# Kernel optimization log

Hardware: AMD Instinct MI355X
Metric: run time of the kernel (lower is better)

Reference implementation:

```python
import jax, jax.numpy as jnp
import numpy as np
from collections import defaultdict

H = 24; W = 24          # patch grid
B0 = 64                 # original batch (len(batch_id))
B = 128                 # total batch incl. augmented copies
C_IN = 256; HID = 128; HEADS_S = 2; OUT = 256; K = 9; NCLS = 8


def _build_space_edges():
    # knn_graph on the normalized meshgrid coords; identical for every image -> offset copies.
    P = H * W
    coords = np.stack(np.meshgrid(np.arange(H), np.arange(W), indexing='ij'), -1).reshape(-1, 2).astype(np.float32)
    cn = coords / coords.max()
    d = ((cn[:, None, :] - cn[None, :, :]) ** 2).sum(-1)
    np.fill_diagonal(d, np.inf)              # loop=False
    nbr = np.argsort(d, axis=1)[:, :K]       # [P, K] neighbor (source) ids
    off = (np.arange(B0) * P)[:, None, None]
    src = (nbr[None] + off).reshape(-1)
    dst = (np.broadcast_to(np.arange(P)[:, None], (P, K))[None] + off).reshape(-1)
    return np.stack([src, dst]).astype(np.int64)


def _build_view_edges(bid_all):
    groups = defaultdict(list)
    for i, c in enumerate(bid_all.tolist()):
        groups[c].append(i)
    ei = []
    for c, mem in groups.items():
        for a in range(len(mem)):
            for b in range(a + 1, len(mem)):
                i, j = mem[a], mem[b]
                if i >= B0 and j >= B0:
                    continue               # skip augmented-augmented pairs
                ei.append((i, j)); ei.append((j, i))
    return np.array(ei, dtype=np.int64).T


def setup_inputs() -> dict:
    key = jax.random.key(0)
    ks = jax.random.split(key, 8)
    bid = np.repeat(np.arange(NCLS), B0 // NCLS).astype(np.int64)
    bid_all = np.concatenate([bid, bid])
    s = 0.05
    return {
        'x': jax.random.normal(ks[0], (B, C_IN, H, W), jnp.float32),
        'batch_id_all': jnp.asarray(bid_all),
        'batch_id': jnp.asarray(bid),
        'edge_index_space': jnp.asarray(_build_space_edges()),
        'edge_index_view': jnp.asarray(_build_view_edges(bid_all)),
        'W_space': jax.random.normal(ks[1], (C_IN, HEADS_S * HID), jnp.float32) * s,
        'att_src_space': jax.random.normal(ks[2], (HEADS_S, HID), jnp.float32) * s,
        'att_dst_space': jax.random.normal(ks[3], (HEADS_S, HID), jnp.float32) * s,
        'bias_space': jnp.zeros((HEADS_S * HID,), jnp.float32),
        'W_view': jax.random.normal(ks[4], (HEADS_S * HID, OUT), jnp.float32) * s,
        'att_src_view': jax.random.normal(ks[5], (1, OUT), jnp.float32) * s,
        'att_dst_view': jax.random.normal(ks[6], (1, OUT), jnp.float32) * s,
        'bias_view': jnp.zeros((OUT,), jnp.float32),
    }


def _gat(xn, edges, Wm, a_src, a_dst, bias, heads, outc):
    # PyG GATConv: linear -> per-edge leaky_relu attn -> segment softmax over dst -> scatter-add
    N = xn.shape[0]
    loops = jnp.arange(N, dtype=edges.dtype)              # add_self_loops=True
    src = jnp.concatenate([edges[0], loops])
    dst = jnp.concatenate([edges[1], loops])
    h = (xn @ Wm).reshape(N, heads, outc)                 # [N, H, C]
    a_s = jnp.sum(h * a_src[None], -1)                    # [N, H]
    a_d = jnp.sum(h * a_dst[None], -1)
    e = jax.nn.leaky_relu(a_s[src] + a_d[dst], 0.2)       # [E, H]
    m = jax.ops.segment_max(e, dst, num_segments=N)
    ee = jnp.exp(e - m[dst])
    ssum = jax.ops.segment_sum(ee, dst, num_segments=N)
    alpha = ee / (ssum[dst] + 1e-16)
    out = jax.ops.segment_sum(h[src] * alpha[..., None], dst, num_segments=N)
    return out.reshape(N, heads * outc) + bias            # concat=True


def reference(x, batch_id_all, batch_id, edge_index_space, edge_index_view,
              W_space, att_src_space, att_dst_space, bias_space,
              W_view, att_src_view, att_dst_view, bias_view):
    P = H * W
    node = x[:B0].transpose(0, 2, 3, 1).reshape(-1, C_IN)                # [B0*P, C_in]
    x_space = _gat(node, edge_index_space, W_space, att_src_space,
                   att_dst_space, bias_space, HEADS_S, HID)              # [B0*P, 256]
    emb = x_space.reshape(B0, P, -1).mean(axis=1)                        # per-image mean pool
    emb_all = emb[jnp.arange(B) % B0]                                    # augmented i -> i % B0
    feat = _gat(emb_all, edge_index_view, W_view, att_src_view,
                att_dst_view, bias_view, 1, OUT)                         # [B, 256]
    C = feat.shape[1]
    x_view = 0.5 * x_space.reshape(B0, P, C) + 0.5 * feat[:B0][:, None, :]
    # torch does .reshape(-1, C).view(B, C, H, W): a raw row-major reinterpret
    return x_view.reshape(B0, C, H, W)
```

## Files before the change

### kernel.cpp

```cpp
#include <hip/hip_runtime.h>

#define PGRID 576
#define NB0   64
#define CIN   256
#define KNN   9
#define NNODE (NB0 * PGRID)

typedef __attribute__((ext_vector_type(8))) short short8;
typedef __attribute__((ext_vector_type(4))) float f32x4;

__device__ __forceinline__ float bf2f(unsigned short u) {
    union { unsigned int i; float f; } v; v.i = ((unsigned int)u) << 16; return v.f;
}
__device__ __forceinline__ unsigned short f2b(float f) {
    unsigned int u = __float_as_uint(f);
    return (unsigned short)((u + 0x7FFFu + ((u >> 16) & 1u)) >> 16);
}

__global__ __launch_bounds__(256) void prep_w(const float* __restrict__ W,
                                              unsigned short* __restrict__ Wt) {
    __shared__ float tile[64][65];
    const int c0 = blockIdx.x * 64, j0 = blockIdx.y * 64;
    const int t = threadIdx.x, lo = t % 64, hi = t / 64;
#pragma unroll
    for (int r = 0; r < 16; ++r)
        tile[r * 4 + hi][lo] = W[(size_t)(c0 + r * 4 + hi) * 256 + j0 + lo];
    __syncthreads();
#pragma unroll
    for (int r = 0; r < 16; ++r)
        Wt[(size_t)(j0 + r * 4 + hi) * 256 + c0 + lo] = f2b(tile[lo][r * 4 + hi]);
}

__global__ __launch_bounds__(256) void gemm_fused(
    const float* __restrict__ x, const unsigned short* __restrict__ Wt,
    const float* __restrict__ att_src, const float* __restrict__ att_dst,
    unsigned short* __restrict__ h, float* __restrict__ as_, float* __restrict__ ad_) {
    const int bx = blockIdx.x;
    const int t  = threadIdx.x;
    const int b  = bx / 9;
    const int p0 = (bx % 9) * 64;
    const int n0 = bx * 64;
    const int l = t & 63, w = t >> 6;
    const int l4 = l >> 4, l15 = l & 15;
    const float* xb = x + (size_t)b * (CIN * PGRID);
    const int prow = p0 + w * 16 + l15;

    float a0[64];
#pragma unroll
    for (int cq = 0; cq < 8; ++cq)
#pragma unroll
        for (int jj = 0; jj < 8; ++jj) {
            int c = cq * 32 + l4 * 8 + jj;
            a0[cq * 8 + jj] = xb[(size_t)c * PGRID + prow];
        }
    short8 apk[8];
#pragma unroll
    for (int cq = 0; cq < 8; ++cq) {
        short8 v;
#pragma unroll
        for (int jj = 0; jj < 8; ++jj) v[jj] = (short)f2b(a0[cq * 8 + jj]);
        apk[cq] = v;
    }

    f32x4 acc[16] = {};
    const unsigned short* wbase = Wt + (size_t)l15 * 256 + l4 * 8;
#pragma unroll
    for (int q = 0; q < 8; ++q) {
#pragma unroll
        for (int f = 0; f < 16; ++f) {
            short8 wf = *(const short8*)(wbase + (size_t)f * 4096 + q * 32);
            acc[f] = __builtin_amdgcn_mfma_f32_16x16x32_bf16(wf, apk[q], acc[f], 0, 0, 0);
        }
    }

    unsigned short* hrow = h + (size_t)(n0 + w * 16 + l15) * 256 + l4 * 4;
#pragma unroll
    for (int f = 0; f < 16; ++f) {
        uint2 pk;
        pk.x = (unsigned int)f2b(acc[f][0]) | ((unsigned int)f2b(acc[f][1]) << 16);
        pk.y = (unsigned int)f2b(acc[f][2]) | ((unsigned int)f2b(acc[f][3]) << 16);
        *(uint2*)(hrow + f * 16) = pk;
    }

    float s0 = 0.f, s1 = 0.f, d0 = 0.f, d1 = 0.f;
#pragma unroll
    for (int f = 0; f < 16; ++f) {
        float4 av = *(const float4*)(att_src + f * 16 + l4 * 4);
        float4 dv = *(const float4*)(att_dst + f * 16 + l4 * 4);
        float ss = acc[f][0] * av.x + acc[f][1] * av.y + acc[f][2] * av.z + acc[f][3] * av.w;
        float dd = acc[f][0] * dv.x + acc[f][1] * dv.y + acc[f][2] * dv.z + acc[f][3] * dv.w;
        if (f < 8) { s0 += ss; d0 += dd; } else { s1 += ss; d1 += dd; }
    }
    s0 += __shfl_xor(s0, 16); s0 += __shfl_xor(s0, 32);
    s1 += __shfl_xor(s1, 16); s1 += __shfl_xor(s1, 32);
    d0 += __shfl_xor(d0, 16); d0 += __shfl_xor(d0, 32);
    d1 += __shfl_xor(d1, 16); d1 += __shfl_xor(d1, 32);
    if (l < 16) {
        int n = n0 + w * 16 + l;
        float2 sv; sv.x = s0; sv.y = s1;
        float2 dv2; dv2.x = d0; dv2.y = d1;
        *(float2*)(as_ + 2 * n) = sv;
        *(float2*)(ad_ + 2 * n) = dv2;
    }
}

__global__ __launch_bounds__(256) void space_gather(
    const unsigned short* __restrict__ h, const float* __restrict__ as_,
    const float* __restrict__ ad_, const int* __restrict__ esrc,
    const float* __restrict__ bias, unsigned short* __restrict__ xsb) {
    const int t = threadIdx.x;
    const int g = t >> 6, l = t & 63;
    const int n = blockIdx.x * 4 + g;
    int srcs[10];
#pragma unroll
    for (int k = 0; k < 9; ++k) srcs[k] = esrc[n * 9 + k];
    srcs[9] = n;
    const int head = l >> 5;
    const float adv = ad_[n * 2 + head];
    float e[10];
    float m = -1e30f;
#pragma unroll
    for (int k = 0; k < 10; ++k) {
        float ev = as_[srcs[k] * 2 + head] + adv;
        ev = ev >= 0.f ? ev : 0.2f * ev;
        e[k] = ev; m = fmaxf(m, ev);
    }
    float ssum = 0.f;
#pragma unroll
    for (int k = 0; k < 10; ++k) { e[k] = __expf(e[k] - m); ssum += e[k]; }
    const float inv = 1.f / (ssum + 1e-16f);
    const int j4 = l * 4;
    float o0 = 0.f, o1 = 0.f, o2 = 0.f, o3 = 0.f;
#pragma unroll
    for (int k = 0; k < 10; ++k) {
        uint2 v = *(const uint2*)(h + (size_t)srcs[k] * 256 + j4);
        o0 += e[k] * bf2f((unsigned short)(v.x & 0xffff));
        o1 += e[k] * bf2f((unsigned short)(v.x >> 16));
        o2 += e[k] * bf2f((unsigned short)(v.y & 0xffff));
        o3 += e[k] * bf2f((unsigned short)(v.y >> 16));
    }
    float4 bi = *(const float4*)(bias + j4);
    o0 = o0 * inv + bi.x; o1 = o1 * inv + bi.y;
    o2 = o2 * inv + bi.z; o3 = o3 * inv + bi.w;
    uint2 pk;
    pk.x = (unsigned int)f2b(o0) | ((unsigned int)f2b(o1) << 16);
    pk.y = (unsigned int)f2b(o2) | ((unsigned int)f2b(o3) << 16);
    *(uint2*)(xsb + (size_t)n * 256 + j4) = pk;
}

__global__ __launch_bounds__(256) void pool_partial(const unsigned short* __restrict__ xsb,
                                                    float* __restrict__ embp) {
    __shared__ float red[4][256];
    const int b = blockIdx.x, seg = blockIdx.y;
    const int t = threadIdx.x;
    const int l = t & 63, sub = t >> 6;
    const int j4 = l * 4;
    const unsigned short* base = xsb + ((size_t)b * PGRID + seg * 64 + sub * 16) * 256 + j4;
    float s0 = 0.f, s1 = 0.f, s2 = 0.f, s3 = 0.f;
#pragma unroll
    for (int p = 0; p < 16; ++p) {
        uint2 v = *(const uint2*)(base + (size_t)p * 256);
        s0 += bf2f((unsigned short)(v.x & 0xffff));
        s1 += bf2f((unsigned short)(v.x >> 16));
        s2 += bf2f((unsigned short)(v.y & 0xffff));
        s3 += bf2f((unsigned short)(v.y >> 16));
    }
    float4 sv; sv.x = s0; sv.y = s1; sv.z = s2; sv.w = s3;
    *(float4*)(&red[sub][j4]) = sv;
    __syncthreads();
    if (sub == 0) {
        float4 a = *(float4*)(&red[1][j4]);
        float4 c = *(float4*)(&red[2][j4]);
        float4 d = *(float4*)(&red[3][j4]);
        float4 r;
        r.x = s0 + a.x + c.x + d.x;
        r.y = s1 + a.y + c.y + d.y;
        r.z = s2 + a.z + c.z + d.z;
        r.w = s3 + a.w + c.w + d.w;
        *(float4*)(embp + ((size_t)b * 9 + seg) * 256 + j4) = r;
    }
}

__global__ __launch_bounds__(256) void view_linear(const float* __restrict__ embp,
                                                   const float* __restrict__ Wv,
                                                   const float* __restrict__ att_s,
                                                   const float* __restrict__ att_d,
                                                   float* __restrict__ hv,
                                                   float* __restrict__ asv,
                                                   float* __restrict__ adv) {
    __shared__ float er[256];
    __shared__ float red[2][256];
    const int i = blockIdx.x;
    const int j = threadIdx.x;
    const int i64 = i & 63;
    float s = 0.f;
#pragma unroll
    for (int seg = 0; seg < 9; ++seg) s += embp[((size_t)i64 * 9 + seg) * 256 + j];
    er[j] = s * (1.f / 576.f);
    __syncthreads();
    float acc = 0.f;
    for (int c = 0; c < 256; ++c) acc += er[c] * Wv[c * 256 + j];
    hv[(size_t)i * 256 + j] = acc;
    red[0][j] = acc * att_s[j];
    red[1][j] = acc * att_d[j];
    __syncthreads();
    for (int off = 128; off > 0; off >>= 1) {
        if (j < off) { red[0][j] += red[0][j + off]; red[1][j] += red[1][j + off]; }
        __syncthreads();
    }
    if (j == 0) { asv[i] = red[0][0]; adv[i] = red[1][0]; }
}

__global__ __launch_bounds__(256) void view_gather(const float* __restrict__ hv,
                                                   const float* __restrict__ asv,
                                                   const float* __restrict__ adv,
                                                   const int* __restrict__ ev,
                                                   int Ev,
                                                   const float* __restrict__ bias,
                                                   float* __restrict__ feat) {
    __shared__ int cnt;
    __shared__ int s_src[32];
    const int d = blockIdx.x;
    const int t = threadIdx.x;
    if (t == 0) cnt = 0;
    __syncthreads();
    for (int e = t; e < Ev; e += 256) {
        if (ev[Ev + e] == d) {
            int pos = atomicAdd(&cnt, 1);
            s_src[pos] = ev[e];
        }
    }
    __syncthreads();
    const int ns = cnt;
    const float adval = adv[d];
    float m = -1e30f;
    float ev_[16];
#pragma unroll 1
    for (int k = 0; k < ns; ++k) {
        float e = asv[s_src[k]] + adval;
        e = e >= 0.f ? e : 0.2f * e;
        ev_[k] = e;
        m = fmaxf(m, e);
    }
    float eself = asv[d] + adval;
    eself = eself >= 0.f ? eself : 0.2f * eself;
    m = fmaxf(m, eself);
    float ssum = 0.f;
#pragma unroll 1
    for (int k = 0; k < ns; ++k) { ev_[k] = __expf(ev_[k] - m); ssum += ev_[k]; }
    float wself = __expf(eself - m);
    ssum += wself;
    const float inv = 1.f / (ssum + 1e-16f);
    float out = 0.f;
#pragma unroll 1
    for (int k = 0; k < ns; ++k) out += ev_[k] * hv[(size_t)s_src[k] * 256 + t];
    out += wself * hv[(size_t)d * 256 + t];
    feat[d * 256 + t] = out * inv + bias[t];
}

__global__ __launch_bounds__(256) void combine(const unsigned short* __restrict__ xsb,
                                               const float* __restrict__ feat,
                                               float* __restrict__ out, int ntot4) {
    int i = blockIdx.x * blockDim.x + threadIdx.x;
    if (i >= ntot4) return;
    size_t f = (size_t)i * 4;
    int b = (int)(f / (PGRID * 256));
    int j = (int)(f & 255);
    uint2 v = *(const uint2*)(xsb + f);
    float4 fb = *(const float4*)(feat + b * 256 + j);
    float4 o;
    o.x = 0.5f * (bf2f((unsigned short)(v.x & 0xffff)) + fb.x);
    o.y = 0.5f * (bf2f((unsigned short)(v.x >> 16))   + fb.y);
    o.z = 0.5f * (bf2f((unsigned short)(v.y & 0xffff)) + fb.z);
    o.w = 0.5f * (bf2f((unsigned short)(v.y >> 16))   + fb.w);
    *(float4*)(out + f) = o;
}

extern "C" void kernel_launch(void* const* d_in, const int* in_sizes, int n_in,
                              void* d_out, int out_size, void* d_ws, size_t ws_size,
                              hipStream_t stream) {
    const float* x        = (const float*)d_in[0];
    const int*   e_space  = (const int*)d_in[3];
    const int*   e_view   = (const int*)d_in[4];
    const float* W_space  = (const float*)d_in[5];
    const float* att_ss   = (const float*)d_in[6];
    const float* att_ds   = (const float*)d_in[7];
    const float* bias_s   = (const float*)d_in[8];
    const float* W_view   = (const float*)d_in[9];
    const float* att_sv   = (const float*)d_in[10];
    const float* att_dv   = (const float*)d_in[11];
    const float* bias_v   = (const float*)d_in[12];
    float* out = (float*)d_out;

    const int Ev = in_sizes[4] / 2;

    char* ws = (char*)d_ws;
    unsigned short* hbf = (unsigned short*)ws;
    unsigned short* Wt  = (unsigned short*)(ws + 18874368);
    unsigned short* xsb = (unsigned short*)(ws + 18874368 + 131072);
    float* as_  = (float*)(ws + 2 * 18874368 + 131072);
    float* ad_  = as_ + NNODE * 2;
    float* embp = ad_ + NNODE * 2;
    float* hv   = embp + 64 * 9 * 256;
    float* asv  = hv  + 128 * 256;
    float* adv  = asv + 128;
    float* feat = adv + 128;

    prep_w<<<dim3(4, 4), 256, 0, stream>>>(W_space, Wt);
    gemm_fused<<<576, 256, 0, stream>>>(x, Wt, att_ss, att_ds, hbf, as_, ad_);
    space_gather<<<NNODE / 4, 256, 0, stream>>>(hbf, as_, ad_, e_space, bias_s, xsb);
    pool_partial<<<dim3(NB0, 9), 256, 0, stream>>>(xsb, embp);
    view_linear<<<128, 256, 0, stream>>>(embp, W_view, att_sv, att_dv, hv, asv, adv);
    view_gather<<<NB0, 256, 0, stream>>>(hv, asv, adv, e_view, Ev, bias_v, feat);

    const int ntot4 = NB0 * PGRID * 256 / 4;
    combine<<<(ntot4 + 255) / 256, 256, 0, stream>>>(xsb, feat, out, ntot4);
}
```

Baseline: 239.8 us.

## Stage GEMM weights through double-buffered swizzled LDS and remap gather block order

The GEMM kernel now stages the bf16 weight matrix in 64-column chunks into a double-buffered LDS area with direct global-to-LDS loads and an XOR swizzle. MFMA operands are then read from LDS instead of from global memory per lane, and the load of the next chunk overlaps compute on the current one. This is meant to cut redundant global/L2 weight traffic and avoid LDS bank conflicts, at the cost of 64KB of LDS per block, which may lower occupancy, plus extra barriers. Separately, the space_gather kernel permutes its block index so consecutive blocks go to different node ranges, likely to spread work across XCDs or improve cache locality.

```diff
diff --git a/kernel.cpp b/kernel.cpp
--- a/kernel.cpp
+++ b/kernel.cpp
@@ -35,6 +35,7 @@
     const float* __restrict__ x, const unsigned short* __restrict__ Wt,
     const float* __restrict__ att_src, const float* __restrict__ att_dst,
     unsigned short* __restrict__ h, float* __restrict__ as_, float* __restrict__ ad_) {
+    __shared__ char ldsB[2][32768];
     const int bx = blockIdx.x;
     const int t  = threadIdx.x;
     const int b  = bx / 9;
@@ -45,6 +46,20 @@
     const float* xb = x + (size_t)b * (CIN * PGRID);
     const int prow = p0 + w * 16 + l15;
 
+#define STAGE_CHUNK(bufsel, ck)                                               \
+    {                                                                         \
+        _Pragma("unroll")                                                     \
+        for (int pass = 0; pass < 8; ++pass) {                                \
+            const int byte_ = pass * 4096 + t * 16;                           \
+            const int j_    = byte_ >> 7;                                     \
+            const int g_    = (byte_ >> 4) & 7;                               \
+            const int gs_   = g_ ^ (j_ & 7);                                  \
+            __builtin_amdgcn_global_load_lds(                                 \
+                (const char*)Wt + (size_t)j_ * 512 + (ck) * 128 + gs_ * 16,   \
+                &ldsB[bufsel][pass * 4096 + (t & 192) * 16], 16, 0, 0);       \
+        }                                                                     \
+    }
+
     float a0[64];
 #pragma unroll
     for (int cq = 0; cq < 8; ++cq)
@@ -53,6 +68,9 @@
             int c = cq * 32 + l4 * 8 + jj;
             a0[cq * 8 + jj] = xb[(size_t)c * PGRID + prow];
         }
+
+    STAGE_CHUNK(0, 0);
+
     short8 apk[8];
 #pragma unroll
     for (int cq = 0; cq < 8; ++cq) {
@@ -63,15 +81,26 @@
     }
 
     f32x4 acc[16] = {};
-    const unsigned short* wbase = Wt + (size_t)l15 * 256 + l4 * 8;
-#pragma unroll
-    for (int q = 0; q < 8; ++q) {
-#pragma unroll
-        for (int f = 0; f < 16; ++f) {
-            short8 wf = *(const short8*)(wbase + (size_t)f * 4096 + q * 32);
-            acc[f] = __builtin_amdgcn_mfma_f32_16x16x32_bf16(wf, apk[q], acc[f], 0, 0, 0);
+    __syncthreads();
+
+#pragma unroll
+    for (int ck = 0; ck < 4; ++ck) {
+        if (ck < 3) STAGE_CHUNK((ck + 1) & 1, ck + 1);
+        const int cur = ck & 1;
+#pragma unroll
+        for (int q = 0; q < 2; ++q) {
+            const int qq = ck * 2 + q;
+#pragma unroll
+            for (int f = 0; f < 16; ++f) {
+                const int j  = f * 16 + l15;
+                const int gs = (q * 4 + l4) ^ (l15 & 7);
+                short8 wf = *(const short8*)&ldsB[cur][j * 128 + gs * 16];
+                acc[f] = __builtin_amdgcn_mfma_f32_16x16x32_bf16(wf, apk[qq], acc[f], 0, 0, 0);
+            }
         }
-    }
+        if (ck < 3) __syncthreads();
+    }
+#undef STAGE_CHUNK
 
     unsigned short* hrow = h + (size_t)(n0 + w * 16 + l15) * 256 + l4 * 4;
 #pragma unroll
@@ -108,9 +137,11 @@
     const unsigned short* __restrict__ h, const float* __restrict__ as_,
     const float* __restrict__ ad_, const int* __restrict__ esrc,
     const float* __restrict__ bias, unsigned short* __restrict__ xsb) {
+    const int orig = blockIdx.x;
+    const int blk  = (orig & 7) * (NNODE / 4 / 8) + (orig >> 3);
     const int t = threadIdx.x;
     const int g = t >> 6, l = t & 63;
-    const int n = blockIdx.x * 4 + g;
+    const int n = blk * 4 + g;
     int srcs[10];
 #pragma unroll
     for (int k = 0; k < 9; ++k) srcs[k] = esrc[n * 9 + k];
```

After: 208.7 us. 1.15x faster.
